# Optimization experiments

Measured on AMD Instinct MI355X. Metric: run time of the kernel, lower is better.

The kernel has to match this reference:

```python
import jax, jax.numpy as jnp
import numpy as np

NTOKENS = 8192
H = 1024
FFN = 2048
NEXPERTS = 64
TOPK = 2
M = NTOKENS * TOPK  # total routed slots


def setup_inputs() -> dict:
    key = jax.random.key(0)
    k1, k2, k3 = jax.random.split(key, 3)
    inputs_shard = jax.random.normal(k1, (NTOKENS, H), dtype=jnp.float32)
    w1 = jax.random.normal(k2, (NEXPERTS, H, FFN), dtype=jnp.float32) * 0.02
    w2 = jax.random.normal(k3, (NEXPERTS, FFN, H), dtype=jnp.float32) * 0.02
    # Balanced routing: each expert receives exactly M // NEXPERTS slots.
    rng = np.random.default_rng(0)
    per_expert = M // NEXPERTS
    eid_flat = rng.permutation(np.repeat(np.arange(M // per_expert), per_expert))  # [M] expert id per (token,k)
    order = np.argsort(eid_flat, kind='stable')  # slot -> flat (token,k) index
    scatter_flat = np.empty(M, dtype=np.int64)
    scatter_flat[order] = np.arange(M)  # (token,k) -> slot in expert-sorted buffer
    scatter_index = jnp.asarray(scatter_flat.reshape(NTOKENS, TOPK))
    splits = jnp.full((NEXPERTS,), per_expert, dtype=jnp.int64)
    return {"inputs_shard": inputs_shard, "w1": w1, "w2": w2,
            "scatter_index": scatter_index, "splits": splits}


def reference(inputs_shard, w1, w2, scatter_index, splits):
    ntokens, topk = scatter_index.shape
    m = ntokens * topk
    nexperts = w1.shape[0]
    per_expert = m // nexperts  # splits are balanced by construction
    # AG-scatter: place each token copy into its expert-sorted slot.
    slot_to_tk = jnp.argsort(scatter_index.reshape(-1))  # slot -> (token,k) flat idx
    token = slot_to_tk // topk                            # slot -> source token
    expanded = inputs_shard[token]                        # [M, H]
    # Grouped GEMM 1 (h -> ffn) + exact gelu, per expert block.
    xg = expanded.reshape(nexperts, per_expert, -1)       # [G, M/G, H]
    h1 = jnp.einsum('geh,ghf->gef', xg, w1)               # [G, M/G, FFN]
    a = jax.nn.gelu(h1, approximate=False)
    # Grouped GEMM 2 (ffn -> h).
    h2 = jnp.einsum('gef,gfh->geh', a, w2).reshape(m, -1)  # [M, H]
    # Gather-RS: gather topk partials per token and reduce (sum).
    out = h2[scatter_index.reshape(-1)].reshape(ntokens, topk, -1).sum(axis=1)
    return out
```

## Files before the change

### kernel.cpp

```cpp
#include <hip/hip_runtime.h>
#include <hip/hip_bf16.h>
#include <math.h>

#define NTOK 8192
#define HD   1024
#define FFND 2048
#define NE   64
#define MTOT 16384
#define PER_E 256

typedef __attribute__((ext_vector_type(8))) short bh8;
typedef __attribute__((ext_vector_type(4))) float f4;
typedef unsigned short u16;
typedef unsigned int   u32;

__device__ __forceinline__ u16 f2bf(float f) {
  union { float f; u32 u; } x; x.f = f;
  u32 r = x.u + 0x7fffu + ((x.u >> 16) & 1u);
  return (u16)(r >> 16);
}

__device__ __forceinline__ u32 pk2(float lo, float hi) {
  __hip_bfloat162 h = __float22bfloat162_rn(make_float2(lo, hi));
  union { __hip_bfloat162 h; u32 u; } c; c.h = h;
  return c.u;
}

__global__ void k_build_s2t(const int* __restrict__ sidx, int* __restrict__ s2t) {
  int i = blockIdx.x * 256 + threadIdx.x;
  s2t[sidx[i]] = i >> 1;
}

__global__ void k_gather_x(const float* __restrict__ inp, const int* __restrict__ s2t,
                           u16* __restrict__ X) {
  int idx = blockIdx.x * 256 + threadIdx.x;
  int slot = idx >> 7;
  int c    = idx & 127;
  const float* src = inp + (size_t)s2t[slot] * HD + c * 8;
  float v[8];
  *(f4*)(v)     = *(const f4*)(src);
  *(f4*)(v + 4) = *(const f4*)(src + 4);
  u32 o[4];
  #pragma unroll
  for (int j = 0; j < 4; ++j) o[j] = pk2(v[2 * j], v[2 * j + 1]);
  *(uint4*)(X + (size_t)slot * HD + c * 8) = *(uint4*)o;
}

template<int K, int N, bool GELU>
__global__ __launch_bounds__(512, 4)
void moe_gemm(const u16* __restrict__ Abf, const float* __restrict__ Bf,
              u16* __restrict__ actout, float* __restrict__ redout)
{
  constexpr int BM = 256, BN = 128, BK = 64;
  constexpr int NB = N / BN;
  __shared__ __align__(16) char lds[BM * 128 + BN * 128];
  char* As = lds;
  char* Bs = lds + BM * 128;

  const int d = blockIdx.y * NB + blockIdx.x;
  const int x = d & 7, j = d >> 3;
  const int e  = x * (NE / 8) + j / NB;
  const int n0 = (j % NB) * BN;
  const int row0 = e * PER_E;
  const int tid  = threadIdx.x;
  const int lane = tid & 63, wid = tid >> 6;
  const int wr   = wid >> 1, wc = wid & 1;

  const u16*   Arow = Abf + (size_t)row0 * K;
  const float* Bsrc = Bf + (size_t)e * K * N + n0;

  f4 acc[4][4] = {};

  for (int k0 = 0; k0 < K; k0 += BK) {
    #pragma unroll
    for (int i = 0; i < 4; ++i) {
      int c = i * 512 + tid;
      int r = c >> 3, kc = c & 7;
      int kswz = kc ^ (r & 7);
      __builtin_amdgcn_global_load_lds(
          (const void*)(Arow + (size_t)r * K + k0 + kswz * 8),
          (void*)(As + c * 16), 16, 0, 0);
    }
    #pragma unroll
    for (int i = 0; i < 2; ++i) {
      int c = i * 512 + tid;
      int n = c & 127, kc = c >> 7;
      const float* p = Bsrc + (size_t)(k0 + kc * 8) * N + n;
      u32 q[4];
      #pragma unroll
      for (int jj = 0; jj < 4; ++jj)
        q[jj] = pk2(p[(size_t)(2 * jj) * N], p[(size_t)(2 * jj + 1) * N]);
      *(uint4*)(Bs + n * 128 + ((kc * 16) ^ ((n & 7) << 4))) = *(uint4*)q;
    }
    __syncthreads();
    #pragma unroll
    for (int kk = 0; kk < 2; ++kk) {
      int kByte = kk * 64 + ((lane >> 4) << 4);
      bh8 a[4], b[4];
      #pragma unroll
      for (int m = 0; m < 4; ++m) {
        int r = wr * 64 + m * 16 + (lane & 15);
        a[m] = *(bh8*)(As + r * 128 + (kByte ^ ((r & 7) << 4)));
      }
      #pragma unroll
      for (int n = 0; n < 4; ++n) {
        int r = wc * 64 + n * 16 + (lane & 15);
        b[n] = *(bh8*)(Bs + r * 128 + (kByte ^ ((r & 7) << 4)));
      }
      #pragma unroll
      for (int m = 0; m < 4; ++m)
        #pragma unroll
        for (int n = 0; n < 4; ++n)
          acc[m][n] = __builtin_amdgcn_mfma_f32_16x16x32_bf16(a[m], b[n], acc[m][n], 0, 0, 0);
    }
    __syncthreads();
  }

  #pragma unroll
  for (int m = 0; m < 4; ++m) {
    #pragma unroll
    for (int n = 0; n < 4; ++n) {
      int rowb = wr * 64 + m * 16 + ((lane >> 4) << 2);
      int col  = n0 + wc * 64 + n * 16 + (lane & 15);
      #pragma unroll
      for (int jj = 0; jj < 4; ++jj) {
        float xv = acc[m][n][jj];
        if (GELU) {
          float y = fminf(fmaxf(xv, -8.f), 8.f);
          float u = 0.7978845608f * (y + 0.044715f * y * y * y);
          float t = __expf(-2.f * u);
          float g = __fdividef(y, 1.f + t);
          actout[(size_t)(row0 + rowb + jj) * N + col] = f2bf(g);
        } else {
          redout[(size_t)(row0 + rowb + jj) * N + col] = xv;
        }
      }
    }
  }
}

__global__ void k_reduce(const float* __restrict__ h2, const int* __restrict__ sidx,
                         float* __restrict__ out) {
  int t = blockIdx.x;
  int c = threadIdx.x;
  const f4* r0 = (const f4*)(h2 + (size_t)sidx[2 * t] * HD);
  const f4* r1 = (const f4*)(h2 + (size_t)sidx[2 * t + 1] * HD);
  ((f4*)(out + (size_t)t * HD))[c] = r0[c] + r1[c];
}

extern "C" void kernel_launch(void* const* d_in, const int* in_sizes, int n_in,
                              void* d_out, int out_size, void* d_ws, size_t ws_size,
                              hipStream_t stream) {
  const float* inp  = (const float*)d_in[0];
  const float* w1   = (const float*)d_in[1];
  const float* w2   = (const float*)d_in[2];
  const int*   sidx = (const int*)d_in[3];
  float* out = (float*)d_out;

  char* ws   = (char*)d_ws;
  int*   s2t = (int*)ws;
  u16*   X   = (u16*)(ws + (1 << 20));
  u16*   act = (u16*)(ws + (1 << 20) + (32u << 20));
  float* h2  = (float*)(ws + (1 << 20) + (96u << 20));

  k_build_s2t<<<MTOT / 256, 256, 0, stream>>>(sidx, s2t);
  k_gather_x<<<(MTOT * (HD / 8)) / 256, 256, 0, stream>>>(inp, s2t, X);
  moe_gemm<HD, FFND, true><<<dim3(FFND / 128, NE), 512, 0, stream>>>(X, w1, act, nullptr);
  moe_gemm<FFND, HD, false><<<dim3(HD / 128, NE), 512, 0, stream>>>(act, w2, nullptr, h2);
  k_reduce<<<NTOK, 256, 0, stream>>>(h2, sidx, out);
}
```

Before: 315.7 us.

## Double-buffer A tiles and prefetch B into registers in grouped MoE GEMM

The GEMM main loop is restructured into a software pipeline. The next A tile is loaded asynchronously into a second LDS buffer, and the next B tile (fp32 weights) is prefetched into registers while the MFMAs for the current tile run. B is then converted and written to LDS after a barrier. Wave priority is raised around the MFMA block. This hides global load latency behind compute, at the cost of more LDS (a second A buffer), 16 extra registers per thread, and an extra barrier per iteration, which may reduce occupancy.

```diff
diff --git a/kernel.cpp b/kernel.cpp
--- a/kernel.cpp
+++ b/kernel.cpp
@@ -53,9 +53,10 @@
 {
   constexpr int BM = 256, BN = 128, BK = 64;
   constexpr int NB = N / BN;
-  __shared__ __align__(16) char lds[BM * 128 + BN * 128];
-  char* As = lds;
-  char* Bs = lds + BM * 128;
+  constexpr int NT = K / BK;
+  constexpr int ABYTES = BM * 128;
+  __shared__ __align__(16) char lds[2 * ABYTES + BN * 128];
+  char* Bs = lds + 2 * ABYTES;
 
   const int d = blockIdx.y * NB + blockIdx.x;
   const int x = d & 7, j = d >> 3;
@@ -69,9 +70,8 @@
   const u16*   Arow = Abf + (size_t)row0 * K;
   const float* Bsrc = Bf + (size_t)e * K * N + n0;
 
-  f4 acc[4][4] = {};
-
-  for (int k0 = 0; k0 < K; k0 += BK) {
+  auto stageA = [&](int buf, int k0) {
+    char* dst = lds + buf * ABYTES;
     #pragma unroll
     for (int i = 0; i < 4; ++i) {
       int c = i * 512 + tid;
@@ -79,20 +79,50 @@
       int kswz = kc ^ (r & 7);
       __builtin_amdgcn_global_load_lds(
           (const void*)(Arow + (size_t)r * K + k0 + kswz * 8),
-          (void*)(As + c * 16), 16, 0, 0);
-    }
+          (void*)(dst + c * 16), 16, 0, 0);
+    }
+  };
+  auto loadB = [&](float* br, int k0) {
     #pragma unroll
     for (int i = 0; i < 2; ++i) {
       int c = i * 512 + tid;
       int n = c & 127, kc = c >> 7;
       const float* p = Bsrc + (size_t)(k0 + kc * 8) * N + n;
+      #pragma unroll
+      for (int jj = 0; jj < 8; ++jj) br[i * 8 + jj] = p[(size_t)jj * N];
+    }
+  };
+  auto writeB = [&](const float* br) {
+    #pragma unroll
+    for (int i = 0; i < 2; ++i) {
+      int c = i * 512 + tid;
+      int n = c & 127, kc = c >> 7;
       u32 q[4];
       #pragma unroll
-      for (int jj = 0; jj < 4; ++jj)
-        q[jj] = pk2(p[(size_t)(2 * jj) * N], p[(size_t)(2 * jj + 1) * N]);
+      for (int jj = 0; jj < 4; ++jj) q[jj] = pk2(br[i * 8 + 2 * jj], br[i * 8 + 2 * jj + 1]);
       *(uint4*)(Bs + n * 128 + ((kc * 16) ^ ((n & 7) << 4))) = *(uint4*)q;
     }
-    __syncthreads();
+  };
+
+  f4 acc[4][4] = {};
+  float breg[16];
+
+  stageA(0, 0);
+  loadB(breg, 0);
+  writeB(breg);
+  asm volatile("s_waitcnt vmcnt(0) lgkmcnt(0)" ::: "memory");
+  __builtin_amdgcn_sched_barrier(0);
+  __builtin_amdgcn_s_barrier();
+  __builtin_amdgcn_sched_barrier(0);
+
+  int cur = 0;
+  for (int t = 0; t < NT; ++t) {
+    const char* As = lds + cur * ABYTES;
+    if (t + 1 < NT) {
+      stageA(cur ^ 1, (t + 1) * BK);
+      loadB(breg, (t + 1) * BK);
+    }
+    __builtin_amdgcn_s_setprio(1);
     #pragma unroll
     for (int kk = 0; kk < 2; ++kk) {
       int kByte = kk * 64 + ((lane >> 4) << 4);
@@ -100,12 +130,12 @@
       #pragma unroll
       for (int m = 0; m < 4; ++m) {
         int r = wr * 64 + m * 16 + (lane & 15);
-        a[m] = *(bh8*)(As + r * 128 + (kByte ^ ((r & 7) << 4)));
+        a[m] = *(const bh8*)(As + r * 128 + (kByte ^ ((r & 7) << 4)));
       }
       #pragma unroll
       for (int n = 0; n < 4; ++n) {
         int r = wc * 64 + n * 16 + (lane & 15);
-        b[n] = *(bh8*)(Bs + r * 128 + (kByte ^ ((r & 7) << 4)));
+        b[n] = *(const bh8*)(Bs + r * 128 + (kByte ^ ((r & 7) << 4)));
       }
       #pragma unroll
       for (int m = 0; m < 4; ++m)
@@ -113,7 +143,17 @@
         for (int n = 0; n < 4; ++n)
           acc[m][n] = __builtin_amdgcn_mfma_f32_16x16x32_bf16(a[m], b[n], acc[m][n], 0, 0, 0);
     }
-    __syncthreads();
+    __builtin_amdgcn_s_setprio(0);
+    __builtin_amdgcn_s_barrier();
+    __builtin_amdgcn_sched_barrier(0);
+    if (t + 1 < NT) {
+      writeB(breg);
+      asm volatile("s_waitcnt vmcnt(0) lgkmcnt(0)" ::: "memory");
+      __builtin_amdgcn_sched_barrier(0);
+      __builtin_amdgcn_s_barrier();
+      __builtin_amdgcn_sched_barrier(0);
+      cur ^= 1;
+    }
   }
 
   #pragma unroll
@@ -128,8 +168,8 @@
         if (GELU) {
           float y = fminf(fmaxf(xv, -8.f), 8.f);
           float u = 0.7978845608f * (y + 0.044715f * y * y * y);
-          float t = __expf(-2.f * u);
-          float g = __fdividef(y, 1.f + t);
+          float t2 = __expf(-2.f * u);
+          float g = __fdividef(y, 1.f + t2);
           actout[(size_t)(row0 + rowb + jj) * N + col] = f2bf(g);
         } else {
           redout[(size_t)(row0 + rowb + jj) * N + col] = xv;
```

Result: faster. 308.8 us (-2.2%).
